# Performance work log

Measured on AMD Instinct MI355X. Metric: run time of the kernel, lower is better.

Reference implementation:

```python
import jax, jax.numpy as jnp
import numpy as np

NEG_INF = -1e30  # large negative for masking; avoids inf*0 NaNs under softmax


def setup_inputs() -> dict:
    key = jax.random.key(0)
    kq, kk, kv, kd = jax.random.split(key, 4)
    B, H, N, D = 1, 16, 4096, 64
    Q = jax.random.normal(kq, (B, H, N, D), dtype=jnp.float32)
    K = jax.random.normal(kk, (B, H, N, D), dtype=jnp.float32)
    V = jax.random.normal(kv, (B, H, N, D), dtype=jnp.float32)
    document_id = jnp.sort(jax.random.randint(kd, (N,), 0, 16, dtype=jnp.int32))
    return {"Q": Q, "K": K, "V": V, "document_id": document_id}


def reference(Q, K, V, document_id):
    # Q, K, V: [B, H, N, D]; document_id: [N]
    B, H, N, D = Q.shape
    scale = 1.0 / jnp.sqrt(jnp.float32(D))  # flex_attention default scaling
    # document mask: token pairs attend only within the same document
    mask = document_id[:, None] == document_id[None, :]  # [N, N] bool
    scores = jnp.einsum('bhqd,bhkd->bhqk', Q, K) * scale  # [B, H, N, N]
    scores = jnp.where(mask[None, None, :, :], scores, NEG_INF)
    probs = jax.nn.softmax(scores, axis=-1)
    out = jnp.einsum('bhqk,bhkd->bhqd', probs, V)  # [B, H, N, D]
    return out
```

## Files before the change

kernel.cpp:

```cpp
#include <hip/hip_runtime.h>
#include <hip/hip_bf16.h>

typedef __attribute__((ext_vector_type(8))) short short8;
typedef __attribute__((ext_vector_type(4))) float f32x4;
typedef __attribute__((ext_vector_type(4))) unsigned int u32x4;
typedef __attribute__((ext_vector_type(4))) unsigned short u16x4;
typedef unsigned short u16;

#define MFMA16 __builtin_amdgcn_mfma_f32_16x16x32_bf16

__device__ __forceinline__ u16 f2bf(float x) {
    unsigned int u = __builtin_bit_cast(unsigned int, x);
    u = (u + 0x7FFFu + ((u >> 16) & 1u)) >> 16;
    return (u16)u;
}
__device__ __forceinline__ unsigned int cvtpk(float lo, float hi) {
    unsigned int r;
    asm("v_cvt_pk_bf16_f32 %0, %1, %2" : "=v"(r) : "v"(lo), "v"(hi));
    return r;
}

constexpr int N_TOK = 4096;
constexpr int DH = 64;
constexpr int KMAX = 224;
constexpr int KST = 72;
constexpr int VST = 248;
constexpr int NSLOT = 3;
constexpr float SCALE = 0.125f;
constexpr float SHIFT = 8.0f;
constexpr float MASKVAL = -1e30f;

__global__ __launch_bounds__(512, 2)
void doc_attn_v11(const float* __restrict__ Qg, const float* __restrict__ Kg,
                  const float* __restrict__ Vg, const int* __restrict__ doc,
                  float* __restrict__ Out) {
    __shared__ u16 Klds[KMAX][KST];
    __shared__ u16 Vtld[DH][VST];
    __shared__ int bnd[2];

    const int bid = blockIdx.x;
    const int swz = ((bid & 7) << 6) | (bid >> 3);
    const int h = swz >> 5;
    const int dI = (swz >> 1) & 15;
    const int qhalf = swz & 1;
    const int tid = threadIdx.x;
    const int lane = tid & 63;
    const int w = tid >> 6;
    const int l15 = lane & 15;
    const int lg = lane >> 4;

    if (tid == 0) { bnd[0] = N_TOK; bnd[1] = N_TOK; }
    __syncthreads();
    {
        const int i0 = tid * 8;
        int prev = (i0 == 0) ? -1 : doc[i0 - 1];
        #pragma unroll
        for (int j = 0; j < 8; ++j) {
            const int cur = doc[i0 + j];
            if (cur >= dI && prev < dI) bnd[0] = i0 + j;
            if (cur >= dI + 1 && prev < dI + 1) bnd[1] = i0 + j;
            prev = cur;
        }
    }
    __syncthreads();
    const int qs = bnd[0], qe = bnd[1];
    const int len = qe - qs;
    if (len <= 0) return;

    const int nG = (len + 15) >> 4;
    const int nGh = (nG + 1) >> 1;
    const int gBeg = qhalf * nGh;
    const int gEnd = min(nG, gBeg + nGh);
    if (gBeg >= gEnd) return;

    const int src0 = l15 + ((lane & 16) << 1);
    const int src1 = src0 + 16;
    const bool khsel = (lg >> 1) != 0;

    for (int g0 = gBeg; g0 < gEnd; g0 += 8 * NSLOT) {
        short8 aq[NSLOT][2];
        int gid[NSLOT];
        #pragma unroll
        for (int s = 0; s < NSLOT; ++s) {
            const int g = g0 + w + 8 * s;
            gid[s] = (g < gEnd) ? g : -1;
            const int gl = (g < gEnd) ? g : 0;
            const int qrow = min(qs + gl * 16 + l15, N_TOK - 1);
            const float* qp = &Qg[((size_t)h * N_TOK + qrow) * DH + lg * 8];
            #pragma unroll
            for (int kc = 0; kc < 2; ++kc) {
                float4 f0 = *(const float4*)(qp + kc * 32);
                float4 f1 = *(const float4*)(qp + kc * 32 + 4);
                short8 a;
                a[0]=(short)f2bf(f0.x*SCALE); a[1]=(short)f2bf(f0.y*SCALE);
                a[2]=(short)f2bf(f0.z*SCALE); a[3]=(short)f2bf(f0.w*SCALE);
                a[4]=(short)f2bf(f1.x*SCALE); a[5]=(short)f2bf(f1.y*SCALE);
                a[6]=(short)f2bf(f1.z*SCALE); a[7]=(short)f2bf(f1.w*SCALE);
                aq[s][kc] = a;
            }
        }

        f32x4 o_acc[NSLOT][4];
        float lsum[NSLOT];
        #pragma unroll
        for (int s = 0; s < NSLOT; ++s) {
            lsum[s] = 0.f;
            #pragma unroll
            for (int db = 0; db < 4; ++db) o_acc[s][db] = (f32x4){0.f, 0.f, 0.f, 0.f};
        }

        for (int c0 = 0; c0 < len; c0 += KMAX) {
            const int clen = min(KMAX, len - c0);
            const int ctiles = (clen + 31) >> 5;
            const int cl32 = ctiles << 5;

            __syncthreads();

            for (int idx = tid; idx < clen * 16; idx += 512) {
                const int r = idx >> 4, c = (idx & 15) * 4;
                const float4 f = *(const float4*)&Kg[((size_t)h * N_TOK + qs + c0 + r) * DH + c];
                u16x4 o4;
                o4[0] = f2bf(f.x); o4[1] = f2bf(f.y);
                o4[2] = f2bf(f.z); o4[3] = f2bf(f.w);
                *(u16x4*)&Klds[r][c] = o4;
            }
            for (int idx = tid; idx < clen * 16; idx += 512) {
                const int r = idx >> 4, c = (idx & 15) * 4;
                const float4 f = *(const float4*)&Vg[((size_t)h * N_TOK + qs + c0 + r) * DH + c];
                Vtld[c + 0][r] = f2bf(f.x);
                Vtld[c + 1][r] = f2bf(f.y);
                Vtld[c + 2][r] = f2bf(f.z);
                Vtld[c + 3][r] = f2bf(f.w);
            }
            for (int idx = tid; idx < DH * 32; idx += 512) {
                const int d_ = idx >> 5;
                const int col = (clen & ~31) + (idx & 31);
                if (col >= clen && col < cl32) Vtld[d_][col] = 0;
            }
            __syncthreads();

            for (int t = 0; t < ctiles; ++t) {
                const int kb = t << 5;
                short8 bk[2][2];
                #pragma unroll
                for (int kh = 0; kh < 2; ++kh)
                    #pragma unroll
                    for (int kc = 0; kc < 2; ++kc)
                        bk[kh][kc] = *(const short8*)&Klds[kb + kh * 16 + l15][lg * 8 + kc * 32];
                short8 bv[4];
                #pragma unroll
                for (int db = 0; db < 4; ++db)
                    bv[db] = *(const short8*)&Vtld[db * 16 + l15][kb + lg * 8];

                #pragma unroll
                for (int s = 0; s < NSLOT; ++s) {
                    if (gid[s] < 0) continue;
                    f32x4 sa0 = (f32x4){-SHIFT, -SHIFT, -SHIFT, -SHIFT};
                    f32x4 sa1 = (f32x4){-SHIFT, -SHIFT, -SHIFT, -SHIFT};
                    sa0 = MFMA16(bk[0][0], aq[s][0], sa0, 0, 0, 0);
                    sa0 = MFMA16(bk[0][1], aq[s][1], sa0, 0, 0, 0);
                    sa1 = MFMA16(bk[1][0], aq[s][0], sa1, 0, 0, 0);
                    sa1 = MFMA16(bk[1][1], aq[s][1], sa1, 0, 0, 0);

                    float p0[4], p1[4];
                    #pragma unroll
                    for (int i = 0; i < 4; ++i) {
                        const int key0 = kb + lg * 4 + i;
                        const float x0 = (key0 < clen)      ? sa0[i] : MASKVAL;
                        const float x1 = (key0 + 16 < clen) ? sa1[i] : MASKVAL;
                        p0[i] = __expf(x0);
                        p1[i] = __expf(x1);
                        lsum[s] += p0[i] + p1[i];
                    }

                    const unsigned int a0 = cvtpk(p0[0], p0[1]);
                    const unsigned int a1 = cvtpk(p0[2], p0[3]);
                    const unsigned int b0 = cvtpk(p1[0], p1[1]);
                    const unsigned int b1 = cvtpk(p1[2], p1[3]);
                    const unsigned int t00 = __shfl((int)a0, src0);
                    const unsigned int t01 = __shfl((int)a1, src0);
                    const unsigned int t10 = __shfl((int)b0, src0);
                    const unsigned int t11 = __shfl((int)b1, src0);
                    const unsigned int u00 = __shfl((int)a0, src1);
                    const unsigned int u01 = __shfl((int)a1, src1);
                    const unsigned int u10 = __shfl((int)b0, src1);
                    const unsigned int u11 = __shfl((int)b1, src1);
                    u32x4 af;
                    af[0] = khsel ? t10 : t00;
                    af[1] = khsel ? t11 : t01;
                    af[2] = khsel ? u10 : u00;
                    af[3] = khsel ? u11 : u01;
                    const short8 pa = __builtin_bit_cast(short8, af);

                    #pragma unroll
                    for (int db = 0; db < 4; ++db)
                        o_acc[s][db] = MFMA16(bv[db], pa, o_acc[s][db], 0, 0, 0);
                }
            }
        }

        #pragma unroll
        for (int s = 0; s < NSLOT; ++s) {
            if (gid[s] < 0) continue;
            float rs = lsum[s];
            rs += __shfl_xor(rs, 16);
            rs += __shfl_xor(rs, 32);
            const float inv = 1.0f / rs;
            const int qrow = qs + gid[s] * 16 + l15;
            if (qrow < qe) {
                float* op = &Out[((size_t)h * N_TOK + qrow) * DH + lg * 4];
                #pragma unroll
                for (int db = 0; db < 4; ++db) {
                    float4 v;
                    v.x = o_acc[s][db][0] * inv;
                    v.y = o_acc[s][db][1] * inv;
                    v.z = o_acc[s][db][2] * inv;
                    v.w = o_acc[s][db][3] * inv;
                    *(float4*)(op + db * 16) = v;
                }
            }
        }
    }
}

extern "C" void kernel_launch(void* const* d_in, const int* in_sizes, int n_in,
                              void* d_out, int out_size, void* d_ws, size_t ws_size,
                              hipStream_t stream) {
    const float* Q = (const float*)d_in[0];
    const float* K = (const float*)d_in[1];
    const float* V = (const float*)d_in[2];
    const int* doc = (const int*)d_in[3];
    float* out = (float*)d_out;

    doc_attn_v11<<<dim3(512), 512, 0, stream>>>(Q, K, V, doc, out);
}
```

Measured before the change: 43.54 us.

## Prefetch K/V chunk into registers before barrier, raise occupancy, add MFMA priority

Each thread now loads its K and V float4 values for the chunk into registers before the barrier and converts and stores them to LDS afterwards, so global latency can overlap the barrier wait of the previous chunk. Query slots per wave drop from three to two and launch bounds rise to four blocks per CU to cut register pressure and allow more resident waves. s_setprio is raised around MFMA groups, and the packed bf16 conversion asm is replaced by software rounding, which costs more ALU work. The gid/slot mapping in the hidden code has to stay consistent with NSLOT=2 for correctness.

```diff
diff --git a/kernel.cpp b/kernel.cpp
--- a/kernel.cpp
+++ b/kernel.cpp
@@ -14,28 +14,24 @@
     u = (u + 0x7FFFu + ((u >> 16) & 1u)) >> 16;
     return (u16)u;
 }
-__device__ __forceinline__ unsigned int cvtpk(float lo, float hi) {
-    unsigned int r;
-    asm("v_cvt_pk_bf16_f32 %0, %1, %2" : "=v"(r) : "v"(lo), "v"(hi));
-    return r;
-}
 
 constexpr int N_TOK = 4096;
 constexpr int DH = 64;
 constexpr int KMAX = 224;
 constexpr int KST = 72;
 constexpr int VST = 248;
-constexpr int NSLOT = 3;
+constexpr int NSLOT = 2;
+constexpr int SIT = (KMAX + 31) / 32;
 constexpr float SCALE = 0.125f;
 constexpr float SHIFT = 8.0f;
 constexpr float MASKVAL = -1e30f;
 
-__global__ __launch_bounds__(512, 2)
-void doc_attn_v11(const float* __restrict__ Qg, const float* __restrict__ Kg,
+__global__ __launch_bounds__(512, 4)
+void doc_attn_v14(const float* __restrict__ Qg, const float* __restrict__ Kg,
                   const float* __restrict__ Vg, const int* __restrict__ doc,
                   float* __restrict__ Out) {
-    __shared__ u16 Klds[KMAX][KST];
-    __shared__ u16 Vtld[DH][VST];
+    __shared__ __align__(16) u16 Klds[KMAX][KST];
+    __shared__ __align__(16) u16 Vtld[DH][VST];
     __shared__ int bnd[2];
 
     const int bid = blockIdx.x;
@@ -114,23 +110,36 @@
             const int ctiles = (clen + 31) >> 5;
             const int cl32 = ctiles << 5;
 
+            float4 kf[SIT], vf[SIT];
+            #pragma unroll
+            for (int it = 0; it < SIT; ++it) {
+                if (it * 32 < clen) {
+                    const int idx = tid + it * 512;
+                    const int r = idx >> 4, c = (idx & 15) * 4;
+                    const int rr = (r < clen) ? r : (clen - 1);
+                    kf[it] = *(const float4*)&Kg[((size_t)h * N_TOK + qs + c0 + rr) * DH + c];
+                    vf[it] = *(const float4*)&Vg[((size_t)h * N_TOK + qs + c0 + rr) * DH + c];
+                }
+            }
+
             __syncthreads();
 
-            for (int idx = tid; idx < clen * 16; idx += 512) {
-                const int r = idx >> 4, c = (idx & 15) * 4;
-                const float4 f = *(const float4*)&Kg[((size_t)h * N_TOK + qs + c0 + r) * DH + c];
-                u16x4 o4;
-                o4[0] = f2bf(f.x); o4[1] = f2bf(f.y);
-                o4[2] = f2bf(f.z); o4[3] = f2bf(f.w);
-                *(u16x4*)&Klds[r][c] = o4;
-            }
-            for (int idx = tid; idx < clen * 16; idx += 512) {
-                const int r = idx >> 4, c = (idx & 15) * 4;
-                const float4 f = *(const float4*)&Vg[((size_t)h * N_TOK + qs + c0 + r) * DH + c];
-                Vtld[c + 0][r] = f2bf(f.x);
-                Vtld[c + 1][r] = f2bf(f.y);
-                Vtld[c + 2][r] = f2bf(f.z);
-                Vtld[c + 3][r] = f2bf(f.w);
+            #pragma unroll
+            for (int it = 0; it < SIT; ++it) {
+                if (it * 32 < clen) {
+                    const int idx = tid + it * 512;
+                    const int r = idx >> 4, c = (idx & 15) * 4;
+                    if (r < clen) {
+                        u16x4 o4;
+                        o4[0] = f2bf(kf[it].x); o4[1] = f2bf(kf[it].y);
+                        o4[2] = f2bf(kf[it].z); o4[3] = f2bf(kf[it].w);
+                        *(u16x4*)&Klds[r][c] = o4;
+                        Vtld[c + 0][r] = f2bf(vf[it].x);
+                        Vtld[c + 1][r] = f2bf(vf[it].y);
+                        Vtld[c + 2][r] = f2bf(vf[it].z);
+                        Vtld[c + 3][r] = f2bf(vf[it].w);
+                    }
+                }
             }
             for (int idx = tid; idx < DH * 32; idx += 512) {
                 const int d_ = idx >> 5;
@@ -157,10 +166,12 @@
                     if (gid[s] < 0) continue;
                     f32x4 sa0 = (f32x4){-SHIFT, -SHIFT, -SHIFT, -SHIFT};
                     f32x4 sa1 = (f32x4){-SHIFT, -SHIFT, -SHIFT, -SHIFT};
+                    __builtin_amdgcn_s_setprio(1);
                     sa0 = MFMA16(bk[0][0], aq[s][0], sa0, 0, 0, 0);
                     sa0 = MFMA16(bk[0][1], aq[s][1], sa0, 0, 0, 0);
                     sa1 = MFMA16(bk[1][0], aq[s][0], sa1, 0, 0, 0);
                     sa1 = MFMA16(bk[1][1], aq[s][1], sa1, 0, 0, 0);
+                    __builtin_amdgcn_s_setprio(0);
 
                     float p0[4], p1[4];
                     #pragma unroll
@@ -173,10 +184,10 @@
                         lsum[s] += p0[i] + p1[i];
                     }
 
-                    const unsigned int a0 = cvtpk(p0[0], p0[1]);
-                    const unsigned int a1 = cvtpk(p0[2], p0[3]);
-                    const unsigned int b0 = cvtpk(p1[0], p1[1]);
-                    const unsigned int b1 = cvtpk(p1[2], p1[3]);
+                    const unsigned int a0 = (unsigned int)f2bf(p0[0]) | ((unsigned int)f2bf(p0[1]) << 16);
+                    const unsigned int a1 = (unsigned int)f2bf(p0[2]) | ((unsigned int)f2bf(p0[3]) << 16);
+                    const unsigned int b0 = (unsigned int)f2bf(p1[0]) | ((unsigned int)f2bf(p1[1]) << 16);
+                    const unsigned int b1 = (unsigned int)f2bf(p1[2]) | ((unsigned int)f2bf(p1[3]) << 16);
                     const unsigned int t00 = __shfl((int)a0, src0);
                     const unsigned int t01 = __shfl((int)a1, src0);
                     const unsigned int t10 = __shfl((int)b0, src0);
@@ -192,9 +203,11 @@
                     af[3] = khsel ? u11 : u01;
                     const short8 pa = __builtin_bit_cast(short8, af);
 
+                    __builtin_amdgcn_s_setprio(1);
                     #pragma unroll
                     for (int db = 0; db < 4; ++db)
                         o_acc[s][db] = MFMA16(bv[db], pa, o_acc[s][db], 0, 0, 0);
+                    __builtin_amdgcn_s_setprio(0);
                 }
             }
         }
@@ -232,5 +245,5 @@
     const int* doc = (const int*)d_in[3];
     float* out = (float*)d_out;
 
-    doc_attn_v11<<<dim3(512), 512, 0, stream>>>(Q, K, V, doc, out);
+    doc_attn_v14<<<dim3(512), 512, 0, stream>>>(Q, K, V, doc, out);
 }
```

Result: slower. 59.86 us (+37.5%).
